# Kernel tuning notes

Measured on AMD Instinct MI355X. Metric: run time of the kernel, lower is better.

## Reference

```python
import jax, jax.numpy as jnp
import numpy as np

B, N, D_ATOM, HID, L = 32, 64, 5, 256, 9
E = N * N
F_E = 2 * HID + 2  # [h_i, h_j, d^2, edge_attr]


def _gather(x, idx):
    # x: (B, N, D), idx: (B, E) -> (B, E, D)
    return jax.vmap(lambda a, i: a[i])(x, idx)


def _segsum(data, idx, n):
    # per-batch unsorted segment sum over destination node idx
    return jax.vmap(lambda d, i: jax.ops.segment_sum(d, i, num_segments=n))(data, idx)


def _safe_dist(diff):
    # sqrt of squared norm, safe at 0 (masked self-edges) for grads
    return jnp.sqrt(jnp.maximum(jnp.sum(diff ** 2, axis=-1, keepdims=True), 1e-12))


def _remove_mean(x, mask):
    n = jnp.sum(mask, axis=1, keepdims=True)
    return (x - jnp.sum(x, axis=1, keepdims=True) / n) * mask


def setup_inputs() -> dict:
    key = jax.random.key(0)
    ks = iter(jax.random.split(key, 32))

    def W(shape):
        return jax.random.normal(next(ks), shape, jnp.float32) * 0.02

    x_in = jax.random.normal(next(ks), (B, N, 3), jnp.float32)
    h_in = jax.random.uniform(next(ks), (B, N, D_ATOM), dtype=jnp.float32)
    t = jax.random.uniform(next(ks), (B, N, 1), dtype=jnp.float32)
    ii, jj = jnp.meshgrid(jnp.arange(N), jnp.arange(N), indexing='ij')
    edges = jnp.stack([ii.reshape(-1), jj.reshape(-1)], axis=-1).astype(jnp.int32)  # (E,2) all pairs
    edge_indices = jnp.broadcast_to(edges[None], (B, E, 2))
    node_mask = jnp.ones((B, N, 1), jnp.float32)
    em = (edges[:, 0] != edges[:, 1]).astype(jnp.float32)[:, None]  # mask self-edges
    edge_mask = jnp.broadcast_to(em[None], (B, E, 1))
    params = dict(
        win_w=W((D_ATOM + 1, HID)), win_b=jnp.zeros((HID,), jnp.float32),
        wout_w=W((HID, D_ATOM + 1)), wout_b=jnp.zeros((D_ATOM + 1,), jnp.float32),
        we_w1=W((L, F_E, HID)), we_b1=jnp.zeros((L, HID), jnp.float32),
        we_w2=W((L, HID, HID)), we_b2=jnp.zeros((L, HID), jnp.float32),
        attn_w=W((L, HID, 1)), attn_b=jnp.zeros((L, 1), jnp.float32),
        wh_w1=W((L, 2 * HID, HID)), wh_b1=jnp.zeros((L, HID), jnp.float32),
        wh_w2=W((L, HID, HID)), wh_b2=jnp.zeros((L, HID), jnp.float32),
        wx_w1=W((L, F_E, HID)), wx_b1=jnp.zeros((L, HID), jnp.float32),
        wx_w2=W((L, HID, HID)), wx_b2=jnp.zeros((L, HID), jnp.float32),
        wx_w3=W((L, HID, 1)),
    )
    return dict(x_in=x_in, h_in=h_in, t=t, node_mask=node_mask, edge_mask=edge_mask,
                edge_indices=edge_indices, **params)


def reference(x_in, h_in, t, node_mask, edge_mask, edge_indices,
              win_w, win_b, wout_w, wout_b,
              we_w1, we_b1, we_w2, we_b2, attn_w, attn_b,
              wh_w1, wh_b1, wh_w2, wh_b2,
              wx_w1, wx_b1, wx_w2, wx_b2, wx_w3):
    idx_i = edge_indices[..., 0]
    idx_j = edge_indices[..., 1]
    # fixed edge attribute: initial pairwise distance
    d_in = _safe_dist(_gather(x_in, idx_i) - _gather(x_in, idx_j)) * edge_mask
    h0 = jnp.concatenate([h_in, t], axis=-1) @ win_w + win_b

    def block(carry, p):
        x, h = carry
        ew1, eb1, ew2, eb2, aw, ab, hw1, hb1, hw2, hb2, xw1, xb1, xw2, xb2, xw3 = p
        diff = (_gather(x, idx_i) - _gather(x, idx_j)) * edge_mask  # (B,E,3)
        d = _safe_dist(diff)  # (B,E,1)
        feat = jnp.concatenate([_gather(h, idx_i), _gather(h, idx_j), d ** 2, d_in], axis=-1) * edge_mask
        # edge MLP + attention gate, aggregated to node i
        m = jax.nn.silu(jax.nn.silu(feat @ ew1 + eb1) @ ew2 + eb2)
        em_agg = _segsum(jax.nn.sigmoid(m @ aw + ab) * m, idx_i, N)
        h_new = (h + (jax.nn.silu(jnp.concatenate([h, em_agg], axis=-1) @ hw1 + hb1) @ hw2 + hb2)) * node_mask
        # coordinate update (no bias on last layer)
        s = jax.nn.silu(jax.nn.silu(feat @ xw1 + xb1) @ xw2 + xb2) @ xw3  # (B,E,1)
        x_new = (x + _segsum(diff / (d + 1.0) * s, idx_i, N)) * node_mask
        return (x_new, h_new), None

    stacked = (we_w1, we_b1, we_w2, we_b2, attn_w, attn_b,
               wh_w1, wh_b1, wh_w2, wh_b2, wx_w1, wx_b1, wx_w2, wx_b2, wx_w3)
    (x, h), _ = jax.lax.scan(block, (x_in, h0), stacked)
    x_out = _remove_mean((x - x_in) * node_mask, node_mask)
    h_out = ((h @ wout_w + wout_b) * node_mask)[..., :-1]
    return jnp.concatenate([x_out, h_out], axis=-1)
```

## Files before the change

### kernel.cpp

```cpp
#include <hip/hip_runtime.h>
#include <math.h>


#define NB   32
#define NN   64
#define EPB  4096
#define HID  256
#define NL   9

typedef __attribute__((ext_vector_type(8))) short bfrag;
typedef __attribute__((ext_vector_type(4))) float f32x4;
typedef __attribute__((ext_vector_type(2))) float f32x2;

__device__ __forceinline__ float fast_rcp(float x) { return __builtin_amdgcn_rcpf(x); }
__device__ __forceinline__ float silu_f(float x) { return x * fast_rcp(1.f + __expf(-x)); }
__device__ __forceinline__ float sigm_f(float x) { return fast_rcp(1.f + __expf(-x)); }
__device__ __forceinline__ unsigned pk_bf16(float a, float b) {
    unsigned ua = __builtin_bit_cast(unsigned, a); ua = (ua + 0x7fffu + ((ua >> 16) & 1u)) >> 16;
    unsigned ub = __builtin_bit_cast(unsigned, b); ub = (ub + 0x7fffu + ((ub >> 16) & 1u)) >> 16;
    return ua | (ub << 16);
}
__device__ __forceinline__ unsigned pk2(f32x2 v) { return pk_bf16(v.x, v.y); }
__device__ __forceinline__ ushort bf16rne(float x) {
    unsigned u = __builtin_bit_cast(unsigned, x);
    u = (u + 0x7fffu + ((u >> 16) & 1u)) >> 16;
    return (ushort)u;
}
__device__ __forceinline__ float bf16tof(ushort h) {
    unsigned u = ((unsigned)h) << 16;
    return __builtin_bit_cast(float, u);
}
__device__ __forceinline__ f32x2 fma2(f32x2 a, f32x2 b, f32x2 c) {
    return __builtin_elementwise_fma(a, b, c);
}
__device__ __forceinline__ f32x4 fma4(f32x4 a, f32x4 b, f32x4 c) {
    return __builtin_elementwise_fma(a, b, c);
}
__device__ __forceinline__ f32x2 silu2(f32x2 v) {
    f32x2 e = { __expf(-v.x), __expf(-v.y) };
    f32x2 d = e + (f32x2){1.f, 1.f};
    f32x2 r = { fast_rcp(d.x), fast_rcp(d.y) };
    return v * r;
}
__device__ __forceinline__ f32x4 silu4(f32x4 v) {
    f32x4 e = { __expf(-v.x), __expf(-v.y), __expf(-v.z), __expf(-v.w) };
    f32x4 d = e + (f32x4){1.f, 1.f, 1.f, 1.f};
    f32x4 r = { fast_rcp(d.x), fast_rcp(d.y), fast_rcp(d.z), fast_rcp(d.w) };
    return v * r;
}

__global__ void edm_k0_pre(const float* __restrict__ x_in, const float* __restrict__ h_in,
                           const float* __restrict__ t_in,
                           const float* __restrict__ win_w, const float* __restrict__ win_b,
                           float* __restrict__ h0, float* __restrict__ din_ws,
                           float* __restrict__ x0)
{
    int blk = blockIdx.x, tid = threadIdx.x;
    if (blk < NB * NN) {
        int node = blk;
        float acc = win_b[tid];
        #pragma unroll
        for (int k = 0; k < 5; ++k) acc += h_in[node * 5 + k] * win_w[k * HID + tid];
        acc += t_in[node] * win_w[5 * HID + tid];
        h0[node * HID + tid] = acc;
    } else if (blk < NB * NN + 512) {
        int e = (blk - NB * NN) * 256 + tid;
        int b = e >> 12, r = e & 4095, i = r >> 6, j = r & 63;
        const float* xb = x_in + b * NN * 3;
        float d0 = xb[i*3+0] - xb[j*3+0];
        float d1 = xb[i*3+1] - xb[j*3+1];
        float d2 = xb[i*3+2] - xb[j*3+2];
        float ss = d0*d0 + d1*d1 + d2*d2;
        float d  = sqrtf(fmaxf(ss, 1e-12f));
        din_ws[e] = (i != j) ? d : 0.f;
    } else {
        int idx = (blk - (NB * NN + 512)) * 256 + tid;
        if (idx < NB * NN * 3) x0[idx] = x_in[idx];
    }
}

__global__ void edm_k5_prep(const float* __restrict__ we_w2, const float* __restrict__ wx_w2,
                            ushort* __restrict__ W2Te, ushort* __restrict__ W2Tx)
{
    __shared__ float t_s[64][65];
    int blk = blockIdx.x;
    int mat = blk / 144, rem = blk % 144, l = rem >> 4, tile = rem & 15;
    int kt = tile >> 2, nt = tile & 3;
    const float* src = (mat ? wx_w2 : we_w2) + l * HID * HID;
    ushort* dst = (mat ? W2Tx : W2Te) + l * HID * HID;
    int col = threadIdx.x & 63, rg = threadIdx.x >> 6;
    #pragma unroll
    for (int it = 0; it < 16; ++it) {
        int row = rg * 16 + it;
        t_s[row][col] = src[(kt * 64 + row) * HID + nt * 64 + col];
    }
    __syncthreads();
    #pragma unroll
    for (int it = 0; it < 16; ++it) {
        int n = rg * 16 + it;
        dst[(nt * 64 + n) * HID + kt * 64 + col] = bf16rne(t_s[col][n]);
    }
}

__global__ void edm_k5b_prep(const float* __restrict__ we_w1, const float* __restrict__ wx_w1,
                             ushort* __restrict__ W1Th, ushort* __restrict__ W1Tl)
{
    __shared__ float t_s[64][65];
    int blk = blockIdx.x;
    int tile = blk & 15, out = (blk >> 4) & 3, l = blk >> 6;
    int kt = tile >> 2, nt = tile & 3;
    const float* src = ((out >= 2) ? wx_w1 : we_w1) + l * 514 * HID + (out & 1) * 256 * HID;
    size_t doff = ((size_t)(l * 4 + out)) * HID * HID;
    ushort* dh = W1Th + doff;
    ushort* dl = W1Tl + doff;
    int col = threadIdx.x & 63, rg = threadIdx.x >> 6;
    #pragma unroll
    for (int it = 0; it < 16; ++it) {
        int row = rg * 16 + it;
        t_s[row][col] = src[(kt * 64 + row) * HID + nt * 64 + col];
    }
    __syncthreads();
    #pragma unroll
    for (int it = 0; it < 16; ++it) {
        int n = rg * 16 + it;
        float v = t_s[col][n];
        ushort h = bf16rne(v);
        float lo = v - bf16tof(h);
        dh[(nt * 64 + n) * HID + kt * 64 + col] = h;
        dl[(nt * 64 + n) * HID + kt * 64 + col] = bf16rne(lo);
    }
}

__global__ __launch_bounds__(256)
void edm_k1_mfma(const float* __restrict__ h,
                 const ushort* __restrict__ W1Th, const ushort* __restrict__ W1Tl,
                 const float* __restrict__ we_b1, const float* __restrict__ wx_b1,
                 const float* __restrict__ we_w2, const float* __restrict__ we_b2,
                 const float* __restrict__ attn_w, const float* __restrict__ attn_b,
                 float* __restrict__ HeA, float* __restrict__ HeB,
                 float* __restrict__ HxA, float* __restrict__ HxB,
                 float* __restrict__ self_em, int l)
{
    int tid = threadIdx.x;
    if (blockIdx.x == 512) {
        __shared__ float m1s[HID];
        __shared__ float ms[HID];
        __shared__ float wred[4];
        __shared__ float gsh;
        const float* eb1 = we_b1 + l * HID;
        m1s[tid] = silu_f(eb1[tid]);
        __syncthreads();
        const float* W2 = we_w2 + l * HID * HID;
        float acc = we_b2[l * HID + tid];
        for (int k = 0; k < HID; ++k) acc += m1s[k] * W2[k * HID + tid];
        float mv = silu_f(acc);
        ms[tid] = mv;
        float p = mv * attn_w[l * HID + tid];
        #pragma unroll
        for (int off = 32; off > 0; off >>= 1) p += __shfl_down(p, off, 64);
        if ((tid & 63) == 0) wred[tid >> 6] = p;
        __syncthreads();
        if (tid == 0) gsh = sigm_f(wred[0] + wred[1] + wred[2] + wred[3] + attn_b[l]);
        __syncthreads();
        self_em[tid] = gsh * ms[tid];
        return;
    }

    __shared__ __align__(16) ushort Ah_s[16384];
    __shared__ __align__(16) ushort Al_s[16384];

    const int cq = blockIdx.x & 3;
    const int out = (blockIdx.x >> 2) & 3;
    const int ntile = blockIdx.x >> 4;
    const int base = ntile * 64;

    {
        const int c  = tid & 31;
        const int jg = tid >> 5;
        const int k0 = c * 8;
        #pragma unroll
        for (int it = 0; it < 8; ++it) {
            int m = it * 8 + jg;
            f32x4 h0 = *(const f32x4*)&h[(base + m) * HID + k0];
            f32x4 h1 = *(const f32x4*)&h[(base + m) * HID + k0 + 4];
            uint4 phi, plo;
            {
                ushort ax = bf16rne(h0.x), ay = bf16rne(h0.y);
                phi.x = (unsigned)ax | ((unsigned)ay << 16);
                plo.x = pk_bf16(h0.x - bf16tof(ax), h0.y - bf16tof(ay));
            }
            {
                ushort ax = bf16rne(h0.z), ay = bf16rne(h0.w);
                phi.y = (unsigned)ax | ((unsigned)ay << 16);
                plo.y = pk_bf16(h0.z - bf16tof(ax), h0.w - bf16tof(ay));
            }
            {
                ushort ax = bf16rne(h1.x), ay = bf16rne(h1.y);
                phi.z = (unsigned)ax | ((unsigned)ay << 16);
                plo.z = pk_bf16(h1.x - bf16tof(ax), h1.y - bf16tof(ay));
            }
            {
                ushort ax = bf16rne(h1.z), ay = bf16rne(h1.w);
                phi.w = (unsigned)ax | ((unsigned)ay << 16);
                plo.w = pk_bf16(h1.z - bf16tof(ax), h1.w - bf16tof(ay));
            }
            unsigned off = (unsigned)(m * 256 + ((c ^ (m & 7)) * 8));
            *(uint4*)&Ah_s[off] = phi;
            *(uint4*)&Al_s[off] = plo;
        }
    }
    __syncthreads();

    const int w = tid >> 6, lane = tid & 63, quad = lane >> 4, l16 = lane & 15;
    const int col = cq * 64 + w * 16 + l16;
    const ushort* Bh = W1Th + ((size_t)(l * 4 + out)) * HID * HID + (size_t)col * HID;
    const ushort* Bl = W1Tl + ((size_t)(l * 4 + out)) * HID * HID + (size_t)col * HID;

    f32x4 acc[4];
    #pragma unroll
    for (int mt = 0; mt < 4; ++mt) acc[mt] = (f32x4){0.f, 0.f, 0.f, 0.f};

    #pragma unroll
    for (int kt = 0; kt < 8; ++kt) {
        const int kof = kt * 32 + quad * 8;
        const int ch  = (kt * 4 + quad) ^ (l16 & 7);
        bfrag bh = *(const bfrag*)&Bh[kof];
        bfrag bl = *(const bfrag*)&Bl[kof];
        bfrag ahr[4], alr[4];
        #pragma unroll
        for (int mt = 0; mt < 4; ++mt) {
            ahr[mt] = *(const bfrag*)&Ah_s[(mt * 16 + l16) * 256 + ch * 8];
            alr[mt] = *(const bfrag*)&Al_s[(mt * 16 + l16) * 256 + ch * 8];
        }
        #pragma unroll
        for (int mt = 0; mt < 4; ++mt) {
            acc[mt] = __builtin_amdgcn_mfma_f32_16x16x32_bf16(ahr[mt], bh, acc[mt], 0, 0, 0);
            acc[mt] = __builtin_amdgcn_mfma_f32_16x16x32_bf16(ahr[mt], bl, acc[mt], 0, 0, 0);
            acc[mt] = __builtin_amdgcn_mfma_f32_16x16x32_bf16(alr[mt], bh, acc[mt], 0, 0, 0);
        }
    }

    float bias = 0.f;
    if (out == 0) bias = we_b1[l * HID + col];
    else if (out == 2) bias = wx_b1[l * HID + col];
    float* dst = (out == 0) ? HeA : (out == 1) ? HeB : (out == 2) ? HxA : HxB;
    #pragma unroll
    for (int mt = 0; mt < 4; ++mt)
        #pragma unroll
        for (int r = 0; r < 4; ++r)
            dst[(base + mt * 16 + quad * 4 + r) * HID + col] = acc[mt][r] + bias;
}

__global__ __launch_bounds__(256, 4)
void edm_kb_gemm(const float* __restrict__ x_cur, float* __restrict__ x_next,
                 const float* __restrict__ HeA, const float* __restrict__ HeB,
                 const float* __restrict__ HxA, const float* __restrict__ HxB,
                 const float* __restrict__ din_ws,
                 const float* __restrict__ we_w1, const float* __restrict__ we_b1,
                 const float* __restrict__ wx_w1, const float* __restrict__ wx_b1,
                 const ushort* __restrict__ W2Te, const ushort* __restrict__ W2Tx,
                 const float* __restrict__ we_b2, const float* __restrict__ wx_b2,
                 const float* __restrict__ attn_w, const float* __restrict__ attn_b,
                 const float* __restrict__ wx_w3,
                 float* __restrict__ em_agg, int l)
{
    __shared__ __align__(16) ushort A_s[16384];
    __shared__ float red_s[256];
    __shared__ float sc_s[64];
    __shared__ float x_s[192];
    __shared__ float d2_s[64], din_s[64];

    const int tid = threadIdx.x;
    const int blk = blockIdx.x;
    const int p = blk >> 11, bi = blk & 2047, b = bi >> 6, i = bi & 63;

    if (tid < 192) x_s[tid] = x_cur[b * 192 + tid];
    __syncthreads();
    if (tid < 64) {
        int j = tid;
        float d0 = x_s[i*3+0] - x_s[j*3+0];
        float d1 = x_s[i*3+1] - x_s[j*3+1];
        float d2 = x_s[i*3+2] - x_s[j*3+2];
        float ss = d0*d0 + d1*d1 + d2*d2;
        float d  = sqrtf(fmaxf(ss, 1e-12f));
        d2_s[j]  = d * d;
        din_s[j] = din_ws[b * EPB + i * 64 + j];
    }
    __syncthreads();

    {
        const float* W1  = (p ? wx_w1 : we_w1) + l * 514 * HID;
        const float* HA  = (p ? HxA : HeA);
        const float* HB  = (p ? HxB : HeB);
        const float* b1p = (p ? wx_b1 : we_b1) + l * HID;

        const int c  = tid & 31;
        const int jg = tid >> 5;
        const int k0 = c * 8;

        f32x4 ra0 = *(const f32x4*)&HA[(b * 64 + i) * HID + k0];
        f32x4 ra1 = *(const f32x4*)&HA[(b * 64 + i) * HID + k0 + 4];
        f32x4 wa0 = *(const f32x4*)&W1[512 * HID + k0];
        f32x4 wa1 = *(const f32x4*)&W1[512 * HID + k0 + 4];
        f32x4 wb0 = *(const f32x4*)&W1[513 * HID + k0];
        f32x4 wb1 = *(const f32x4*)&W1[513 * HID + k0 + 4];
        f32x4 b10 = *(const f32x4*)&b1p[k0];
        f32x4 b11 = *(const f32x4*)&b1p[k0 + 4];
        uint4 pki;
        pki.x = pk2(silu2((f32x2){b10.x, b10.y}));
        pki.y = pk2(silu2((f32x2){b10.z, b10.w}));
        pki.z = pk2(silu2((f32x2){b11.x, b11.y}));
        pki.w = pk2(silu2((f32x2){b11.z, b11.w}));

        const float* hbp = HB + b * 64 * HID + k0;
        #pragma unroll
        for (int it = 0; it < 8; ++it) {
            int j = it * 8 + jg;
            f32x4 h0 = *(const f32x4*)&hbp[j * HID];
            f32x4 h1 = *(const f32x4*)&hbp[j * HID + 4];
            f32x2 dd = { d2_s[j], d2_s[j] };
            f32x2 dn = { din_s[j], din_s[j] };
            uint4 pkv;
            f32x2 v;
            v = fma2(dn, (f32x2){wb0.x, wb0.y},
                 fma2(dd, (f32x2){wa0.x, wa0.y},
                      (f32x2){ra0.x + h0.x, ra0.y + h0.y}));
            pkv.x = pk2(silu2(v));
            v = fma2(dn, (f32x2){wb0.z, wb0.w},
                 fma2(dd, (f32x2){wa0.z, wa0.w},
                      (f32x2){ra0.z + h0.z, ra0.w + h0.w}));
            pkv.y = pk2(silu2(v));
            v = fma2(dn, (f32x2){wb1.x, wb1.y},
                 fma2(dd, (f32x2){wa1.x, wa1.y},
                      (f32x2){ra1.x + h1.x, ra1.y + h1.y}));
            pkv.z = pk2(silu2(v));
            v = fma2(dn, (f32x2){wb1.z, wb1.w},
                 fma2(dd, (f32x2){wa1.z, wa1.w},
                      (f32x2){ra1.z + h1.z, ra1.w + h1.w}));
            pkv.w = pk2(silu2(v));
            if (j == i) pkv = pki;
            *(uint4*)&A_s[j * 256 + (unsigned)((c ^ (j & 7)) * 8)] = pkv;
        }
    }
    __syncthreads();

    const int w = tid >> 6, lane = tid & 63, quad = lane >> 4, l16 = lane & 15;
    const ushort* W2T = (p ? W2Tx : W2Te) + l * HID * HID;
    const int cb0 = w * 64 + l16;
    f32x4 acc[4][4];
    #pragma unroll
    for (int mt = 0; mt < 4; ++mt)
        #pragma unroll
        for (int nt = 0; nt < 4; ++nt) acc[mt][nt] = (f32x4){0.f, 0.f, 0.f, 0.f};

    #pragma unroll
    for (int kt = 0; kt < 8; ++kt) {
        const int kof = kt * 32 + quad * 8;
        const int ch  = (kt * 4 + quad) ^ (l16 & 7);
        bfrag bfr[4], afr[4];
        #pragma unroll
        for (int nt = 0; nt < 4; ++nt)
            bfr[nt] = *(const bfrag*)&W2T[(cb0 + nt * 16) * HID + kof];
        #pragma unroll
        for (int mt = 0; mt < 4; ++mt)
            afr[mt] = *(const bfrag*)&A_s[(mt * 16 + l16) * 256 + ch * 8];
        #pragma unroll
        for (int mt = 0; mt < 4; ++mt)
            #pragma unroll
            for (int nt = 0; nt < 4; ++nt)
                acc[mt][nt] = __builtin_amdgcn_mfma_f32_16x16x32_bf16(
                    afr[mt], bfr[nt], acc[mt][nt], 0, 0, 0);
    }

    const float* b2p = (p ? wx_b2 : we_b2) + l * HID;
    const float* vvp = p ? (wx_w3 + l * HID) : (attn_w + l * HID);
    float b2v[4], vv[4];
    #pragma unroll
    for (int nt = 0; nt < 4; ++nt) { b2v[nt] = b2p[cb0 + nt * 16]; vv[nt] = vvp[cb0 + nt * 16]; }

    #pragma unroll
    for (int mt = 0; mt < 4; ++mt)
        #pragma unroll
        for (int nt = 0; nt < 4; ++nt) {
            f32x4 bb = { b2v[nt], b2v[nt], b2v[nt], b2v[nt] };
            acc[mt][nt] = silu4(acc[mt][nt] + bb);
        }

    #pragma unroll
    for (int mt = 0; mt < 4; ++mt) {
        f32x4 t4 = acc[mt][0] * (f32x4){vv[0], vv[0], vv[0], vv[0]};
        t4 = fma4(acc[mt][1], (f32x4){vv[1], vv[1], vv[1], vv[1]}, t4);
        t4 = fma4(acc[mt][2], (f32x4){vv[2], vv[2], vv[2], vv[2]}, t4);
        t4 = fma4(acc[mt][3], (f32x4){vv[3], vv[3], vv[3], vv[3]}, t4);
        #pragma unroll
        for (int r = 0; r < 4; ++r) {
            float pd = t4[r];
            pd += __shfl_xor(pd, 1, 64); pd += __shfl_xor(pd, 2, 64);
            pd += __shfl_xor(pd, 4, 64); pd += __shfl_xor(pd, 8, 64);
            if (l16 == 0) red_s[w * 64 + mt * 16 + quad * 4 + r] = pd;
        }
    }
    __syncthreads();
    if (tid < 64) {
        float tot = red_s[tid] + red_s[64 + tid] + red_s[128 + tid] + red_s[192 + tid];
        if (p == 0) sc_s[tid] = (tid == i) ? 0.f : sigm_f(tot + attn_b[l]);
        else        sc_s[tid] = tot;
    }
    __syncthreads();

    if (p == 0) {
        f32x4 g[4];
        #pragma unroll
        for (int mt = 0; mt < 4; ++mt) g[mt] = *(const f32x4*)&sc_s[mt * 16 + quad * 4];
        #pragma unroll
        for (int nt = 0; nt < 4; ++nt) {
            f32x4 e4 = g[0] * acc[0][nt];
            e4 = fma4(g[1], acc[1][nt], e4);
            e4 = fma4(g[2], acc[2][nt], e4);
            e4 = fma4(g[3], acc[3][nt], e4);
            float e = (e4.x + e4.y) + (e4.z + e4.w);
            e += __shfl_xor(e, 16, 64); e += __shfl_xor(e, 32, 64);
            if (quad == 0) em_agg[(b * 64 + i) * HID + cb0 + nt * 16] = e;
        }
    } else {
        if (tid < 64) {
            int j = tid;
            float d0 = x_s[i*3+0] - x_s[j*3+0];
            float d1 = x_s[i*3+1] - x_s[j*3+1];
            float d2 = x_s[i*3+2] - x_s[j*3+2];
            float ss = d0*d0 + d1*d1 + d2*d2;
            float d  = sqrtf(fmaxf(ss, 1e-12f));
            float f  = fast_rcp(d + 1.f) * sc_s[j];
            float cx = d0 * f, cy = d1 * f, cz = d2 * f;
            #pragma unroll
            for (int off = 32; off > 0; off >>= 1) {
                cx += __shfl_down(cx, off, 64);
                cy += __shfl_down(cy, off, 64);
                cz += __shfl_down(cz, off, 64);
            }
            if (tid == 0) {
                x_next[bi * 3 + 0] = x_s[i*3+0] + cx;
                x_next[bi * 3 + 1] = x_s[i*3+1] + cy;
                x_next[bi * 3 + 2] = x_s[i*3+2] + cz;
            }
        }
    }
}

__global__ __launch_bounds__(256)
void edm_k3_nodeupd(const float* __restrict__ h, const float* __restrict__ em_agg,
                    const float* __restrict__ self_em,
                    const float* __restrict__ wh_w1, const float* __restrict__ wh_b1,
                    const float* __restrict__ wh_w2, const float* __restrict__ wh_b2,
                    float* __restrict__ h_next, int l)
{
    __shared__ __align__(16) float cat_s[4][512];
    __shared__ __align__(16) float u_s[4][HID];
    int tid = threadIdx.x;
    int base = blockIdx.x * 4;
    float se = self_em[tid];
    #pragma unroll
    for (int m = 0; m < 4; ++m) {
        cat_s[m][tid]       = h[(base + m) * HID + tid];
        cat_s[m][HID + tid] = em_agg[(base + m) * HID + tid] + se;
    }
    __syncthreads();

    const float* W1 = wh_w1 + l * 512 * HID;
    float b1 = wh_b1[l * HID + tid];
    float acc[4];
    #pragma unroll
    for (int m = 0; m < 4; ++m) acc[m] = b1;
    for (int k = 0; k < 512; k += 4) {
        float w0 = W1[(k + 0) * HID + tid];
        float w1 = W1[(k + 1) * HID + tid];
        float w2 = W1[(k + 2) * HID + tid];
        float w3 = W1[(k + 3) * HID + tid];
        #pragma unroll
        for (int m = 0; m < 4; ++m) {
            float4 a = *(const float4*)&cat_s[m][k];
            acc[m] = fmaf(a.x, w0, fmaf(a.y, w1, fmaf(a.z, w2, fmaf(a.w, w3, acc[m]))));
        }
    }
    #pragma unroll
    for (int m = 0; m < 4; ++m) u_s[m][tid] = silu_f(acc[m]);
    __syncthreads();

    const float* W2 = wh_w2 + l * HID * HID;
    float b2 = wh_b2[l * HID + tid];
    #pragma unroll
    for (int m = 0; m < 4; ++m) acc[m] = b2;
    for (int k = 0; k < HID; k += 4) {
        float w0 = W2[(k + 0) * HID + tid];
        float w1 = W2[(k + 1) * HID + tid];
        float w2 = W2[(k + 2) * HID + tid];
        float w3 = W2[(k + 3) * HID + tid];
        #pragma unroll
        for (int m = 0; m < 4; ++m) {
            float4 a = *(const float4*)&u_s[m][k];
            acc[m] = fmaf(a.x, w0, fmaf(a.y, w1, fmaf(a.z, w2, fmaf(a.w, w3, acc[m]))));
        }
    }
    #pragma unroll
    for (int m = 0; m < 4; ++m)
        h_next[(base + m) * HID + tid] = cat_s[m][tid] + acc[m];
}

__global__ void edm_k4_out(const float* __restrict__ x_fin, const float* __restrict__ x_in,
                           const float* __restrict__ h_fin,
                           const float* __restrict__ wout_w, const float* __restrict__ wout_b,
                           float* __restrict__ out)
{
    __shared__ float vx[192];
    __shared__ float mean_s[3];
    int b = blockIdx.x, tid = threadIdx.x;
    if (tid < 192) vx[tid] = x_fin[b * 192 + tid] - x_in[b * 192 + tid];
    __syncthreads();
    if (tid < 3) {
        float s = 0.f;
        for (int n = 0; n < 64; ++n) s += vx[n * 3 + tid];
        mean_s[tid] = s * (1.f / 64.f);
    }
    __syncthreads();
    if (tid < 192) out[b * 512 + (tid / 3) * 8 + (tid % 3)] = vx[tid] - mean_s[tid % 3];

    int node = tid / 5, ch = tid % 5;
    float acc = wout_b[ch];
    const float* hr = h_fin + (b * 64 + node) * HID;
    for (int k = 0; k < HID; ++k) acc = fmaf(hr[k], wout_w[k * 6 + ch], acc);
    out[b * 512 + node * 8 + 3 + ch] = acc;
}

extern "C" void kernel_launch(void* const* d_in, const int* in_sizes, int n_in,
                              void* d_out, int out_size, void* d_ws, size_t ws_size,
                              hipStream_t stream)
{
    const float* x_in   = (const float*)d_in[0];
    const float* h_in   = (const float*)d_in[1];
    const float* t_in   = (const float*)d_in[2];
    const float* win_w  = (const float*)d_in[6];
    const float* win_b  = (const float*)d_in[7];
    const float* wout_w = (const float*)d_in[8];
    const float* wout_b = (const float*)d_in[9];
    const float* we_w1  = (const float*)d_in[10];
    const float* we_b1  = (const float*)d_in[11];
    const float* we_w2  = (const float*)d_in[12];
    const float* we_b2  = (const float*)d_in[13];
    const float* attn_w = (const float*)d_in[14];
    const float* attn_b = (const float*)d_in[15];
    const float* wh_w1  = (const float*)d_in[16];
    const float* wh_b1  = (const float*)d_in[17];
    const float* wh_w2  = (const float*)d_in[18];
    const float* wh_b2  = (const float*)d_in[19];
    const float* wx_w1  = (const float*)d_in[20];
    const float* wx_b1  = (const float*)d_in[21];
    const float* wx_w2  = (const float*)d_in[22];
    const float* wx_b2  = (const float*)d_in[23];
    const float* wx_w3  = (const float*)d_in[24];

    float* ws = (float*)d_ws;
    const size_t SN = (size_t)NB * NN * HID;
    float* h_a = ws;
    float* h_b = ws + SN;
    float* HeA = ws + 2 * SN;
    float* HeB = ws + 3 * SN;
    float* HxA = ws + 4 * SN;
    float* HxB = ws + 5 * SN;
    float* emg = ws + 6 * SN;
    float* din = ws + 7 * SN;
    float* x_a = din + (size_t)NB * EPB;
    float* x_b = x_a + NB * NN * 3;
    float* sem = x_b + NB * NN * 3;
    ushort* W2Te = (ushort*)(sem + 256);
    ushort* W2Tx = W2Te + (size_t)NL * HID * HID;
    ushort* W1Th = W2Tx + (size_t)NL * HID * HID;
    ushort* W1Tl = W1Th + (size_t)NL * 4 * HID * HID;

    edm_k5_prep<<<dim3(288), dim3(256), 0, stream>>>(we_w2, wx_w2, W2Te, W2Tx);
    edm_k5b_prep<<<dim3(576), dim3(256), 0, stream>>>(we_w1, wx_w1, W1Th, W1Tl);

    edm_k0_pre<<<dim3(NB * NN + 512 + 24), dim3(256), 0, stream>>>(
        x_in, h_in, t_in, win_w, win_b, h_a, din, x_a);

    for (int l = 0; l < NL; ++l) {
        float* h_cur = (l & 1) ? h_b : h_a;
        float* h_nxt = (l & 1) ? h_a : h_b;
        float* x_cur = (l & 1) ? x_b : x_a;
        float* x_nxt = (l & 1) ? x_a : x_b;

        edm_k1_mfma<<<dim3(513), dim3(256), 0, stream>>>(
            h_cur, W1Th, W1Tl, we_b1, wx_b1, we_w2, we_b2, attn_w, attn_b,
            HeA, HeB, HxA, HxB, sem, l);

        edm_kb_gemm<<<dim3(2 * NB * NN), dim3(256), 0, stream>>>(
            x_cur, x_nxt, HeA, HeB, HxA, HxB, din,
            we_w1, we_b1, wx_w1, wx_b1, W2Te, W2Tx,
            we_b2, wx_b2, attn_w, attn_b, wx_w3, emg, l);

        edm_k3_nodeupd<<<dim3(512), dim3(256), 0, stream>>>(
            h_cur, emg, sem, wh_w1, wh_b1, wh_w2, wh_b2, h_nxt, l);
    }

    edm_k4_out<<<dim3(NB), dim3(320), 0, stream>>>(
        x_b, x_in, h_b, wout_w, wout_b, (float*)d_out);
}
```

Measured before the change: 1.232 ms.

## Move node-update MLP to split-bf16 MFMA with pre-transposed weights

Replaces the scalar FP32 node-update kernel (4 nodes per block, 512 blocks) with an MFMA kernel that handles 16 nodes per block. It uses a bf16 hi/lo split (three MFMAs per tile) to keep near-FP32 accuracy. A new prep kernel transposes and splits wh_w1/wh_w2 into bf16 hi/lo arrays once per call. It also swaps the hand-written bf16 pack for the HIP intrinsic conversion. The risks are fewer blocks (128), which lowers parallelism, and extra workspace needed for the weights.

```diff
diff --git a/kernel.cpp b/kernel.cpp
--- a/kernel.cpp
+++ b/kernel.cpp
@@ -1,4 +1,5 @@
 #include <hip/hip_runtime.h>
+#include <hip/hip_bf16.h>
 #include <math.h>
 
 
@@ -15,12 +16,6 @@
 __device__ __forceinline__ float fast_rcp(float x) { return __builtin_amdgcn_rcpf(x); }
 __device__ __forceinline__ float silu_f(float x) { return x * fast_rcp(1.f + __expf(-x)); }
 __device__ __forceinline__ float sigm_f(float x) { return fast_rcp(1.f + __expf(-x)); }
-__device__ __forceinline__ unsigned pk_bf16(float a, float b) {
-    unsigned ua = __builtin_bit_cast(unsigned, a); ua = (ua + 0x7fffu + ((ua >> 16) & 1u)) >> 16;
-    unsigned ub = __builtin_bit_cast(unsigned, b); ub = (ub + 0x7fffu + ((ub >> 16) & 1u)) >> 16;
-    return ua | (ub << 16);
-}
-__device__ __forceinline__ unsigned pk2(f32x2 v) { return pk_bf16(v.x, v.y); }
 __device__ __forceinline__ ushort bf16rne(float x) {
     unsigned u = __builtin_bit_cast(unsigned, x);
     u = (u + 0x7fffu + ((u >> 16) & 1u)) >> 16;
@@ -29,6 +24,13 @@
 __device__ __forceinline__ float bf16tof(ushort h) {
     unsigned u = ((unsigned)h) << 16;
     return __builtin_bit_cast(float, u);
+}
+__device__ __forceinline__ unsigned pk2(f32x2 v) {
+    float2 f; f.x = v.x; f.y = v.y;
+    __hip_bfloat162 t = __float22bfloat162_rn(f);
+    unsigned u;
+    __builtin_memcpy(&u, &t, 4);
+    return u;
 }
 __device__ __forceinline__ f32x2 fma2(f32x2 a, f32x2 b, f32x2 c) {
     return __builtin_elementwise_fma(a, b, c);
@@ -131,6 +133,45 @@
     }
 }
 
+__global__ void edm_k5c_prep(const float* __restrict__ wh_w1, const float* __restrict__ wh_w2,
+                             ushort* __restrict__ W3h, ushort* __restrict__ W3l,
+                             ushort* __restrict__ W4h, ushort* __restrict__ W4l)
+{
+    __shared__ float t_s[64][65];
+    int blk = blockIdx.x;
+    const float* src; ushort* dh; ushort* dl; int kt, nt, Kdim;
+    if (blk < 288) {
+        int l = blk >> 5, tile = blk & 31;
+        kt = tile >> 2; nt = tile & 3; Kdim = 512;
+        src = wh_w1 + (size_t)l * 512 * HID;
+        dh = W3h + (size_t)l * HID * 512;
+        dl = W3l + (size_t)l * HID * 512;
+    } else {
+        int b2 = blk - 288;
+        int l = b2 >> 4, tile = b2 & 15;
+        kt = tile >> 2; nt = tile & 3; Kdim = 256;
+        src = wh_w2 + (size_t)l * HID * HID;
+        dh = W4h + (size_t)l * HID * HID;
+        dl = W4l + (size_t)l * HID * HID;
+    }
+    int col = threadIdx.x & 63, rg = threadIdx.x >> 6;
+    #pragma unroll
+    for (int it = 0; it < 16; ++it) {
+        int row = rg * 16 + it;
+        t_s[row][col] = src[(size_t)(kt * 64 + row) * HID + nt * 64 + col];
+    }
+    __syncthreads();
+    #pragma unroll
+    for (int it = 0; it < 16; ++it) {
+        int n = rg * 16 + it;
+        float v = t_s[col][n];
+        ushort h = bf16rne(v);
+        float lo = v - bf16tof(h);
+        dh[(size_t)(nt * 64 + n) * Kdim + kt * 64 + col] = h;
+        dl[(size_t)(nt * 64 + n) * Kdim + kt * 64 + col] = bf16rne(lo);
+    }
+}
+
 __global__ __launch_bounds__(256)
 void edm_k1_mfma(const float* __restrict__ h,
                  const ushort* __restrict__ W1Th, const ushort* __restrict__ W1Tl,
@@ -187,22 +228,22 @@
             {
                 ushort ax = bf16rne(h0.x), ay = bf16rne(h0.y);
                 phi.x = (unsigned)ax | ((unsigned)ay << 16);
-                plo.x = pk_bf16(h0.x - bf16tof(ax), h0.y - bf16tof(ay));
+                plo.x = pk2((f32x2){h0.x - bf16tof(ax), h0.y - bf16tof(ay)});
             }
             {
                 ushort ax = bf16rne(h0.z), ay = bf16rne(h0.w);
                 phi.y = (unsigned)ax | ((unsigned)ay << 16);
-                plo.y = pk_bf16(h0.z - bf16tof(ax), h0.w - bf16tof(ay));
+                plo.y = pk2((f32x2){h0.z - bf16tof(ax), h0.w - bf16tof(ay)});
             }
             {
                 ushort ax = bf16rne(h1.x), ay = bf16rne(h1.y);
                 phi.z = (unsigned)ax | ((unsigned)ay << 16);
-                plo.z = pk_bf16(h1.x - bf16tof(ax), h1.y - bf16tof(ay));
+                plo.z = pk2((f32x2){h1.x - bf16tof(ax), h1.y - bf16tof(ay)});
             }
             {
                 ushort ax = bf16rne(h1.z), ay = bf16rne(h1.w);
                 phi.w = (unsigned)ax | ((unsigned)ay << 16);
-                plo.w = pk_bf16(h1.z - bf16tof(ax), h1.w - bf16tof(ay));
+                plo.w = pk2((f32x2){h1.z - bf16tof(ax), h1.w - bf16tof(ay)});
             }
             unsigned off = (unsigned)(m * 256 + ((c ^ (m & 7)) * 8));
             *(uint4*)&Ah_s[off] = phi;
@@ -448,62 +489,139 @@
 }
 
 __global__ __launch_bounds__(256)
-void edm_k3_nodeupd(const float* __restrict__ h, const float* __restrict__ em_agg,
-                    const float* __restrict__ self_em,
-                    const float* __restrict__ wh_w1, const float* __restrict__ wh_b1,
-                    const float* __restrict__ wh_w2, const float* __restrict__ wh_b2,
-                    float* __restrict__ h_next, int l)
-{
-    __shared__ __align__(16) float cat_s[4][512];
-    __shared__ __align__(16) float u_s[4][HID];
-    int tid = threadIdx.x;
-    int base = blockIdx.x * 4;
-    float se = self_em[tid];
-    #pragma unroll
-    for (int m = 0; m < 4; ++m) {
-        cat_s[m][tid]       = h[(base + m) * HID + tid];
-        cat_s[m][HID + tid] = em_agg[(base + m) * HID + tid] + se;
-    }
-    __syncthreads();
-
-    const float* W1 = wh_w1 + l * 512 * HID;
-    float b1 = wh_b1[l * HID + tid];
-    float acc[4];
-    #pragma unroll
-    for (int m = 0; m < 4; ++m) acc[m] = b1;
-    for (int k = 0; k < 512; k += 4) {
-        float w0 = W1[(k + 0) * HID + tid];
-        float w1 = W1[(k + 1) * HID + tid];
-        float w2 = W1[(k + 2) * HID + tid];
-        float w3 = W1[(k + 3) * HID + tid];
-        #pragma unroll
-        for (int m = 0; m < 4; ++m) {
-            float4 a = *(const float4*)&cat_s[m][k];
-            acc[m] = fmaf(a.x, w0, fmaf(a.y, w1, fmaf(a.z, w2, fmaf(a.w, w3, acc[m]))));
-        }
-    }
-    #pragma unroll
-    for (int m = 0; m < 4; ++m) u_s[m][tid] = silu_f(acc[m]);
-    __syncthreads();
-
-    const float* W2 = wh_w2 + l * HID * HID;
-    float b2 = wh_b2[l * HID + tid];
-    #pragma unroll
-    for (int m = 0; m < 4; ++m) acc[m] = b2;
-    for (int k = 0; k < HID; k += 4) {
-        float w0 = W2[(k + 0) * HID + tid];
-        float w1 = W2[(k + 1) * HID + tid];
-        float w2 = W2[(k + 2) * HID + tid];
-        float w3 = W2[(k + 3) * HID + tid];
-        #pragma unroll
-        for (int m = 0; m < 4; ++m) {
-            float4 a = *(const float4*)&u_s[m][k];
-            acc[m] = fmaf(a.x, w0, fmaf(a.y, w1, fmaf(a.z, w2, fmaf(a.w, w3, acc[m]))));
-        }
-    }
-    #pragma unroll
-    for (int m = 0; m < 4; ++m)
-        h_next[(base + m) * HID + tid] = cat_s[m][tid] + acc[m];
+void edm_k3_mfma(const float* __restrict__ h, const float* __restrict__ em_agg,
+                 const float* __restrict__ self_em,
+                 const ushort* __restrict__ W3h, const ushort* __restrict__ W3l,
+                 const float* __restrict__ wh_b1,
+                 const ushort* __restrict__ W4h, const ushort* __restrict__ W4l,
+                 const float* __restrict__ wh_b2,
+                 float* __restrict__ h_next, int l)
+{
+    __shared__ __align__(16) ushort Ah_s[16 * 512];
+    __shared__ __align__(16) ushort Al_s[16 * 512];
+    __shared__ __align__(16) ushort Uh_s[16 * 256];
+    __shared__ __align__(16) ushort Ul_s[16 * 256];
+
+    const int tid = threadIdx.x;
+    const int base = blockIdx.x * 16;
+
+    {
+        const int c  = tid & 63;
+        const int jg = tid >> 6;
+        const int k0 = c * 8;
+        #pragma unroll
+        for (int t = 0; t < 4; ++t) {
+            int m = t * 4 + jg;
+            f32x4 v0, v1;
+            if (c < 32) {
+                v0 = *(const f32x4*)&h[(base + m) * HID + k0];
+                v1 = *(const f32x4*)&h[(base + m) * HID + k0 + 4];
+            } else {
+                int e0 = k0 - 256;
+                f32x4 a0 = *(const f32x4*)&em_agg[(base + m) * HID + e0];
+                f32x4 a1 = *(const f32x4*)&em_agg[(base + m) * HID + e0 + 4];
+                f32x4 s0 = *(const f32x4*)&self_em[e0];
+                f32x4 s1 = *(const f32x4*)&self_em[e0 + 4];
+                v0 = a0 + s0; v1 = a1 + s1;
+            }
+            uint4 phi, plo;
+            {
+                ushort ax = bf16rne(v0.x), ay = bf16rne(v0.y);
+                phi.x = (unsigned)ax | ((unsigned)ay << 16);
+                plo.x = pk2((f32x2){v0.x - bf16tof(ax), v0.y - bf16tof(ay)});
+            }
+            {
+                ushort ax = bf16rne(v0.z), ay = bf16rne(v0.w);
+                phi.y = (unsigned)ax | ((unsigned)ay << 16);
+                plo.y = pk2((f32x2){v0.z - bf16tof(ax), v0.w - bf16tof(ay)});
+            }
+            {
+                ushort ax = bf16rne(v1.x), ay = bf16rne(v1.y);
+                phi.z = (unsigned)ax | ((unsigned)ay << 16);
+                plo.z = pk2((f32x2){v1.x - bf16tof(ax), v1.y - bf16tof(ay)});
+            }
+            {
+                ushort ax = bf16rne(v1.z), ay = bf16rne(v1.w);
+                phi.w = (unsigned)ax | ((unsigned)ay << 16);
+                plo.w = pk2((f32x2){v1.z - bf16tof(ax), v1.w - bf16tof(ay)});
+            }
+            unsigned off = (unsigned)(m * 512 + ((c ^ (m & 7)) * 8));
+            *(uint4*)&Ah_s[off] = phi;
+            *(uint4*)&Al_s[off] = plo;
+        }
+    }
+    __syncthreads();
+
+    const int w = tid >> 6, lane = tid & 63, quad = lane >> 4, l16 = lane & 15;
+
+    f32x4 acc1[4];
+    #pragma unroll
+    for (int nt = 0; nt < 4; ++nt) acc1[nt] = (f32x4){0.f, 0.f, 0.f, 0.f};
+
+    for (int ks = 0; ks < 16; ++ks) {
+        const int kof = ks * 32 + quad * 8;
+        unsigned aoff = (unsigned)(l16 * 512 + (((ks * 4 + quad) ^ (l16 & 7))) * 8);
+        bfrag ah = *(const bfrag*)&Ah_s[aoff];
+        bfrag al = *(const bfrag*)&Al_s[aoff];
+        #pragma unroll
+        for (int nt = 0; nt < 4; ++nt) {
+            int col = w * 64 + nt * 16 + l16;
+            bfrag bh = *(const bfrag*)&W3h[((size_t)l * HID + col) * 512 + kof];
+            bfrag bl = *(const bfrag*)&W3l[((size_t)l * HID + col) * 512 + kof];
+            acc1[nt] = __builtin_amdgcn_mfma_f32_16x16x32_bf16(ah, bh, acc1[nt], 0, 0, 0);
+            acc1[nt] = __builtin_amdgcn_mfma_f32_16x16x32_bf16(ah, bl, acc1[nt], 0, 0, 0);
+            acc1[nt] = __builtin_amdgcn_mfma_f32_16x16x32_bf16(al, bh, acc1[nt], 0, 0, 0);
+        }
+    }
+
+    #pragma unroll
+    for (int nt = 0; nt < 4; ++nt) {
+        int colv = w * 64 + nt * 16 + l16;
+        float b1v = wh_b1[l * HID + colv];
+        #pragma unroll
+        for (int r = 0; r < 4; ++r) {
+            float u = silu_f(acc1[nt][r] + b1v);
+            ushort uh = bf16rne(u);
+            float ulo = u - bf16tof(uh);
+            int row = quad * 4 + r;
+            unsigned ao = (unsigned)(row * 256 + (((colv >> 3) ^ (row & 7))) * 8 + (colv & 7));
+            Uh_s[ao] = uh;
+            Ul_s[ao] = bf16rne(ulo);
+        }
+    }
+    __syncthreads();
+
+    f32x4 acc2[4];
+    #pragma unroll
+    for (int nt = 0; nt < 4; ++nt) acc2[nt] = (f32x4){0.f, 0.f, 0.f, 0.f};
+
+    #pragma unroll
+    for (int kt = 0; kt < 8; ++kt) {
+        const int kof = kt * 32 + quad * 8;
+        unsigned aoff = (unsigned)(l16 * 256 + (((kt * 4 + quad) ^ (l16 & 7))) * 8);
+        bfrag ah = *(const bfrag*)&Uh_s[aoff];
+        bfrag al = *(const bfrag*)&Ul_s[aoff];
+        #pragma unroll
+        for (int nt = 0; nt < 4; ++nt) {
+            int col = w * 64 + nt * 16 + l16;
+            bfrag bh = *(const bfrag*)&W4h[((size_t)l * HID + col) * HID + kof];
+            bfrag bl = *(const bfrag*)&W4l[((size_t)l * HID + col) * HID + kof];
+            acc2[nt] = __builtin_amdgcn_mfma_f32_16x16x32_bf16(ah, bh, acc2[nt], 0, 0, 0);
+            acc2[nt] = __builtin_amdgcn_mfma_f32_16x16x32_bf16(ah, bl, acc2[nt], 0, 0, 0);
+            acc2[nt] = __builtin_amdgcn_mfma_f32_16x16x32_bf16(al, bh, acc2[nt], 0, 0, 0);
+        }
+    }
+
+    #pragma unroll
+    for (int nt = 0; nt < 4; ++nt) {
+        int colv = w * 64 + nt * 16 + l16;
+        float b2v = wh_b2[l * HID + colv];
+        #pragma unroll
+        for (int r = 0; r < 4; ++r) {
+            int node = base + quad * 4 + r;
+            h_next[node * HID + colv] = h[node * HID + colv] + acc2[nt][r] + b2v;
+        }
+    }
 }
 
 __global__ void edm_k4_out(const float* __restrict__ x_fin, const float* __restrict__ x_in,
@@ -575,9 +693,14 @@
     ushort* W2Tx = W2Te + (size_t)NL * HID * HID;
     ushort* W1Th = W2Tx + (size_t)NL * HID * HID;
     ushort* W1Tl = W1Th + (size_t)NL * 4 * HID * HID;
+    ushort* W3h  = W1Tl + (size_t)NL * 4 * HID * HID;
+    ushort* W3l  = W3h + (size_t)NL * HID * 512;
+    ushort* W4h  = W3l + (size_t)NL * HID * 512;
+    ushort* W4l  = W4h + (size_t)NL * HID * HID;
 
     edm_k5_prep<<<dim3(288), dim3(256), 0, stream>>>(we_w2, wx_w2, W2Te, W2Tx);
     edm_k5b_prep<<<dim3(576), dim3(256), 0, stream>>>(we_w1, wx_w1, W1Th, W1Tl);
+    edm_k5c_prep<<<dim3(432), dim3(256), 0, stream>>>(wh_w1, wh_w2, W3h, W3l, W4h, W4l);
 
     edm_k0_pre<<<dim3(NB * NN + 512 + 24), dim3(256), 0, stream>>>(
         x_in, h_in, t_in, win_w, win_b, h_a, din, x_a);
@@ -597,8 +720,8 @@
             we_w1, we_b1, wx_w1, wx_b1, W2Te, W2Tx,
             we_b2, wx_b2, attn_w, attn_b, wx_w3, emg, l);
 
-        edm_k3_nodeupd<<<dim3(512), dim3(256), 0, stream>>>(
-            h_cur, emg, sem, wh_w1, wh_b1, wh_w2, wh_b2, h_nxt, l);
+        edm_k3_mfma<<<dim3(128), dim3(256), 0, stream>>>(
+            h_cur, emg, sem, W3h, W3l, wh_b1, W4h, W4l, wh_b2, h_nxt, l);
     }
 
     edm_k4_out<<<dim3(NB), dim3(320), 0, stream>>>(
```

Result: slower. 1.273 ms (+3.3%).
